# Performance work log

Hardware: AMD Instinct MI355X
Metric: run time of the kernel (lower is better)

## Reference

```python
import jax, jax.numpy as jnp
import numpy as np

Z_LOSS_COEF = 0.001
TOP_K = 8


def setup_inputs() -> dict:
    key = jax.random.key(0)
    ks = jax.random.split(key, 8)
    D, L, E, F, FS = 1024, 256, 64, 256, 1024  # d_model, latent, experts, latent d_ff, shared d_ff
    B, S = 1, 1024
    x = jax.random.normal(ks[0], (B, S, D), jnp.float32)
    gate_w = jax.random.normal(ks[1], (E, D), jnp.float32) * 0.01  # router, std=0.01 init
    expert_bias = jnp.zeros((E,), jnp.float32)  # load-balancing bias buffer
    down_w = jax.random.normal(ks[2], (L, D), jnp.float32) * 0.02
    up_w = jax.random.normal(ks[3], (D, L), jnp.float32) * 0.02
    shared_gu_w = jax.random.normal(ks[4], (2 * FS, D), jnp.float32) * 0.02
    shared_down_w = jax.random.normal(ks[5], (D, FS), jnp.float32) * 0.02
    exp_gu_w = jax.random.normal(ks[6], (E, L, 2 * F), jnp.float32) * 0.02  # [E,K,N] layout
    exp_down_w = jax.random.normal(ks[7], (E, F, L), jnp.float32) * 0.02
    return {"x": x, "gate_w": gate_w, "expert_bias": expert_bias,
            "down_w": down_w, "up_w": up_w,
            "shared_gu_w": shared_gu_w, "shared_down_w": shared_down_w,
            "exp_gu_w": exp_gu_w, "exp_down_w": exp_down_w}


def reference(x, gate_w, expert_bias, down_w, up_w, shared_gu_w, shared_down_w, exp_gu_w, exp_down_w):
    B, S, D = x.shape
    xf = x.reshape(-1, D)                     # [N, D]
    N = xf.shape[0]
    E = gate_w.shape[0]
    # ---- AuxLossFreeRouter (full d_model input) ----
    logits = xf @ gate_w.T                    # [N, E]
    z_loss = Z_LOSS_COEF * jnp.mean(jax.nn.logsumexp(logits, axis=-1) ** 2)
    affinity = jax.nn.sigmoid(logits)
    scores = affinity + expert_bias           # bias only affects selection, not weights
    _, sel = jax.lax.top_k(scores, TOP_K)     # [N, K] int32
    sel_aff = jnp.take_along_axis(affinity, sel, axis=1)
    gw = sel_aff / (sel_aff.sum(-1, keepdims=True) + 1e-9)  # [N, K]
    # sparse combine matrix [N, E]
    combine = jnp.zeros((N, E), xf.dtype).at[jnp.arange(N)[:, None], sel].add(gw)
    # ---- shared SwiGLU expert at full d_model ----
    sh = xf @ shared_gu_w.T
    g, u = jnp.split(sh, 2, axis=-1)
    shared_out = (jax.nn.silu(g) * u) @ shared_down_w.T     # [N, D]
    # ---- latent batched experts: down-project, dense-over-E SwiGLU, sparse combine ----
    lat = xf @ down_w.T                       # [N, L]
    h = jnp.einsum('nl,elf->nef', lat, exp_gu_w)            # [N, E, 2F]
    hg, hu = jnp.split(h, 2, axis=-1)
    hid = jax.nn.silu(hg) * hu                # [N, E, F]
    y = jnp.einsum('nef,efl->nel', hid, exp_down_w)         # [N, E, L]
    routed_lat = jnp.einsum('ne,nel->nl', combine, y)       # sparse top-k combine
    routed = routed_lat @ up_w.T              # [N, D]
    out = (shared_out + routed).reshape(B, S, D)
    return out, z_loss
```

## Files before the change

### kernel.cpp

```cpp
#include <hip/hip_runtime.h>
#include <stdint.h>


using f32x4 = __attribute__((ext_vector_type(4))) float;
using s16x8 = __attribute__((ext_vector_type(8))) short;

#define MFMA_BF16(a, b, c) __builtin_amdgcn_mfma_f32_16x16x32_bf16((a), (b), (c), 0, 0, 0)

__device__ __forceinline__ unsigned short f2bf(float f) {
  union { float f; uint32_t u; } v; v.f = f;
  uint32_t u = v.u;
  u += 0x7FFFu + ((u >> 16) & 1u);
  return (unsigned short)(u >> 16);
}
__device__ __forceinline__ float bf2f(unsigned short h) {
  union { uint32_t u; float f; } v; v.u = ((uint32_t)h) << 16;
  return v.f;
}
__device__ __forceinline__ float silu_f(float x) { return x / (1.f + expf(-x)); }

__device__ __forceinline__ void cvt16(const float* __restrict__ src,
                                      unsigned short* __restrict__ dst) {
  if (src) {
#pragma unroll
    for (int i = 0; i < 4; ++i) {
      float4 v = *(const float4*)(src + i * 4);
      *(ushort4*)(dst + i * 4) =
          make_ushort4(f2bf(v.x), f2bf(v.y), f2bf(v.z), f2bf(v.w));
    }
  } else {
#pragma unroll
    for (int i = 0; i < 4; ++i) *(ushort4*)(dst + i * 4) = make_ushort4(0, 0, 0, 0);
  }
}

struct PackArgs {
  const float *x, *gate, *down, *sgu, *sdw, *up, *egu, *edw;
  unsigned short *xb, *Wcat, *Bf, *egut, *edwt;
  int* counts;
  float* zp;
};

__global__ void pack_kernel(PackArgs a) {
  __shared__ float tile[32][33];
  const int b = blockIdx.x, t = threadIdx.x;
  if (b == 0) {
    if (t < 64) a.counts[t] = 0;
    if (t == 64) *a.zp = 0.f;
  }
  if (b < 608) {
    const int r = b * 4 + (t >> 6), c = (t & 63) * 16;
    const float* src;
    if (r < 64)       src = a.gate + (size_t)r * 1024 + c;
    else if (r < 320) src = a.down + (size_t)(r - 64) * 1024 + c;
    else if (r < 384) src = nullptr;
    else {
      const int i = r - 384;
      src = a.sgu + (size_t)((i >> 1) + (i & 1) * 1024) * 1024 + c;
    }
    cvt16(src, a.Wcat + (size_t)r * 1024 + c);
  } else if (b < 928) {
    const int idx = (b - 608) * 4096 + t * 16;
    const int row = idx / 1280, col = idx - row * 1280;
    const float* src = (col < 1024) ? a.sdw + (size_t)row * 1024 + col
                                    : a.up + (size_t)row * 256 + (col - 1024);
    cvt16(src, a.Bf + idx);
  } else if (b < 1184) {
    const int idx = (b - 928) * 4096 + t * 16;
    cvt16(a.x + idx, a.xb + idx);
  } else {
    const float* src; unsigned short* dst; int lds, tr, tc; bool inter;
    if (b < 9376) {
      const int q = b - 1184, e = q >> 7, tt = q & 127;
      tr = tt >> 4; tc = tt & 15; lds = 512; inter = true;
      src = a.egu + (size_t)e * 131072; dst = a.egut + (size_t)e * 131072;
    } else {
      const int q = b - 9376, e = q >> 6, tt = q & 63;
      tr = tt >> 3; tc = tt & 7; lds = 256; inter = false;
      src = a.edw + (size_t)e * 65536; dst = a.edwt + (size_t)e * 65536;
    }
    const int r = t >> 3, c4 = (t & 7) * 4;
    float4 v = *(const float4*)(src + (size_t)(tr * 32 + r) * lds + tc * 32 + c4);
    tile[r][c4 + 0] = v.x; tile[r][c4 + 1] = v.y;
    tile[r][c4 + 2] = v.z; tile[r][c4 + 3] = v.w;
    __syncthreads();
    const int n = tc * 32 + r;
    const int orow = inter ? ((n < 256) ? 2 * n : 2 * (n - 256) + 1) : n;
    ushort4 o = make_ushort4(f2bf(tile[c4 + 0][r]), f2bf(tile[c4 + 1][r]),
                             f2bf(tile[c4 + 2][r]), f2bf(tile[c4 + 3][r]));
    *(ushort4*)(dst + (size_t)orow * 256 + tr * 32 + c4) = o;
  }
}

struct EpiArgs { int mode; void* out; int ldo; int coff; };

__device__ __forceinline__ void stage_tile(const unsigned short* __restrict__ G, int ldg,
                                           int row0, int kt, unsigned short* lbuf,
                                           int wid, int lane) {
#pragma unroll
  for (int j = 0; j < 2; ++j) {
    const int o = j * 4096 + wid * 1024 + lane * 16;
    const int kh = o >> 11;
    const int row = (o & 2047) >> 4;
    const unsigned short* src = G + (size_t)(row0 + row) * ldg + kt * 32 + kh * 8;
    __builtin_amdgcn_global_load_lds(
        (const __attribute__((address_space(1))) void*)src,
        (__attribute__((address_space(3))) void*)(lbuf + (size_t)(j * 2048 + wid * 512)),
        16, 0, 0);
  }
}

__device__ __forceinline__ void wave_fence() { asm volatile("" ::: "memory"); }

__device__ __forceinline__ void gemm_tile(const unsigned short* __restrict__ A, int lda,
                                          const unsigned short* __restrict__ B, int ldb,
                                          int K, int m0, int n0, EpiArgs epi,
                                          unsigned short* As, unsigned short* Bs) {
  const int tid = threadIdx.x;
  const int wid = tid >> 6, lane = tid & 63;
  const int wm = wid >> 1, wn = wid & 1;

  f32x4 acc[4][4] = {};
  const int NT = K >> 5;

  stage_tile(A, lda, m0, 0, As, wid, lane);
  stage_tile(B, ldb, n0, 0, Bs, wid, lane);
  if (NT > 1) {
    stage_tile(A, lda, m0, 1, As + 4096, wid, lane);
    stage_tile(B, ldb, n0, 1, Bs + 4096, wid, lane);
  }

  const int kh = lane >> 4, r16 = lane & 15;
  int cur = 0;
  for (int kt = 0; kt < NT; ++kt) {
    if (kt + 1 < NT) asm volatile("s_waitcnt vmcnt(4)" ::: "memory");
    else             asm volatile("s_waitcnt vmcnt(0)" ::: "memory");
    wave_fence();
    __builtin_amdgcn_s_barrier();
    wave_fence();

    const unsigned short* Ab = As + cur * 4096;
    const unsigned short* Bb = Bs + cur * 4096;
    s16x8 af[4], bfr[4];
#pragma unroll
    for (int m = 0; m < 4; ++m)
      af[m] = *(const s16x8*)(Ab + kh * 1024 + (wm * 64 + m * 16 + r16) * 8);
#pragma unroll
    for (int n = 0; n < 4; ++n)
      bfr[n] = *(const s16x8*)(Bb + kh * 1024 + (wn * 64 + n * 16 + r16) * 8);

    if (kt + 2 < NT) {
      const int nb = (cur + 2 >= 3) ? cur - 1 : cur + 2;
      stage_tile(A, lda, m0, kt + 2, As + nb * 4096, wid, lane);
      stage_tile(B, ldb, n0, kt + 2, Bs + nb * 4096, wid, lane);
    }

    __builtin_amdgcn_s_setprio(1);
#pragma unroll
    for (int m = 0; m < 4; ++m)
#pragma unroll
      for (int n = 0; n < 4; ++n)
        acc[m][n] = MFMA_BF16(af[m], bfr[n], acc[m][n]);
    __builtin_amdgcn_s_setprio(0);

    cur = (cur + 1 == 3) ? 0 : cur + 1;
  }

#pragma unroll
  for (int m = 0; m < 4; ++m) {
    const int rb = m0 + wm * 64 + m * 16 + (lane >> 4) * 4;
#pragma unroll
    for (int n = 0; n < 4; ++n) {
      const int c = n0 + wn * 64 + n * 16 + (lane & 15);
      if (epi.mode == 0) {
        float* O = (float*)epi.out;
#pragma unroll
        for (int j = 0; j < 4; ++j) O[(size_t)(rb + j) * epi.ldo + c] = acc[m][n][j];
      } else if (epi.mode == 1) {
        unsigned short* O = (unsigned short*)epi.out;
#pragma unroll
        for (int j = 0; j < 4; ++j)
          O[(size_t)(rb + j) * epi.ldo + c] = f2bf(acc[m][n][j]);
      } else {
        unsigned short* O = (unsigned short*)epi.out;
        const int col = (c - epi.coff) >> 1;
#pragma unroll
        for (int j = 0; j < 4; ++j) {
          const float v = acc[m][n][j];
          const float u = __shfl_xor(v, 1);
          if (!(lane & 1))
            O[(size_t)(rb + j) * epi.ldo + col] = f2bf(silu_f(v) * u);
        }
      }
    }
  }
}

__global__ __launch_bounds__(256, 1) void gemm1_kernel(const unsigned short* __restrict__ xb,
                                                       const unsigned short* __restrict__ Wcat,
                                                       float* __restrict__ C1,
                                                       unsigned short* __restrict__ Abuf) {
  __shared__ __align__(16) unsigned short As[3 * 4096];
  __shared__ __align__(16) unsigned short Bs[3 * 4096];
  const int bx = blockIdx.x;
  EpiArgs e;
  if (bx < 3) { e.mode = 0; e.out = C1; e.ldo = 384; e.coff = 0; }
  else        { e.mode = 2; e.out = Abuf; e.ldo = 1280; e.coff = 384; }
  gemm_tile(xb, 1024, Wcat, 1024, 1024, blockIdx.y * 128, bx * 128, e, As, Bs);
}

__global__ __launch_bounds__(256, 1) void gemm_final(const unsigned short* __restrict__ Abuf,
                                                     const unsigned short* __restrict__ Bf,
                                                     float* __restrict__ out) {
  __shared__ __align__(16) unsigned short As[3 * 4096];
  __shared__ __align__(16) unsigned short Bs[3 * 4096];
  EpiArgs e; e.mode = 0; e.out = out; e.ldo = 1024; e.coff = 0;
  gemm_tile(Abuf, 1280, Bf, 1280, 1280, blockIdx.y * 128, blockIdx.x * 128, e, As, Bs);
}

__global__ __launch_bounds__(256, 1) void gemm_grouped(const unsigned short* __restrict__ A0,
                                                       const unsigned short* __restrict__ B0,
                                                       int Bstride, EpiArgs epi, int K,
                                                       const int* __restrict__ counts) {
  const int e = blockIdx.y >> 1, rt = blockIdx.y & 1;
  int cnt = counts[e];
  if (cnt > 256) cnt = 256;
  if (rt * 128 >= cnt) return;
  __shared__ __align__(16) unsigned short As[3 * 4096];
  __shared__ __align__(16) unsigned short Bs[3 * 4096];
  const int base = e * 256 + rt * 128;
  epi.out = (void*)((unsigned short*)epi.out + (size_t)base * epi.ldo);
  gemm_tile(A0 + (size_t)base * K, K, B0 + (size_t)e * Bstride, K, K, 0,
            blockIdx.x * 128, epi, As, Bs);
}

__global__ void router_kernel(const float* __restrict__ C1,
                              const float* __restrict__ bias,
                              unsigned short* __restrict__ lat_g,
                              int* __restrict__ counts,
                              int* __restrict__ slot_nk, float* __restrict__ gw_nk,
                              float* __restrict__ zp) {
  const int n = blockIdx.x * 4 + (threadIdx.x >> 6);
  const int lane = threadIdx.x & 63;
  const float* row = C1 + (size_t)n * 384;
  const float logit = row[lane];

  float mx = logit;
#pragma unroll
  for (int d = 32; d; d >>= 1) mx = fmaxf(mx, __shfl_xor(mx, d));
  float se = expf(logit - mx);
#pragma unroll
  for (int d = 32; d; d >>= 1) se += __shfl_xor(se, d);
  if (lane == 0) {
    const float lse = mx + logf(se);
    atomicAdd(zp, 0.001f * lse * lse * (1.f / 1024.f));
  }

  const float aff = 1.f / (1.f + expf(-logit));
  float s = aff + bias[lane];

  float asum = 0.f;
  int e_mine = 0; float a_mine = 0.f;
#pragma unroll
  for (int k = 0; k < 8; ++k) {
    float m2 = s;
#pragma unroll
    for (int d = 32; d; d >>= 1) m2 = fmaxf(m2, __shfl_xor(m2, d));
    const unsigned long long blt = __ballot(s == m2);
    const int idx = __ffsll(blt) - 1;
    const float a = __shfl(aff, idx);
    asum += a;
    if (lane == k) { e_mine = idx; a_mine = a; }
    if (lane == idx) s = -3.0e38f;
  }
  const float inv = 1.f / (asum + 1e-9f);

  int slot = 0;
  if (lane < 8) {
    int pos = atomicAdd(&counts[e_mine], 1);
    if (pos > 255) pos = 255;
    slot = e_mine * 256 + pos;
    slot_nk[(size_t)n * 8 + lane] = slot;
    gw_nk[(size_t)n * 8 + lane] = a_mine * inv;
  }

  const float4 lv = *(const float4*)(row + 64 + lane * 4);
  const ushort4 lb = make_ushort4(f2bf(lv.x), f2bf(lv.y), f2bf(lv.z), f2bf(lv.w));
#pragma unroll
  for (int k = 0; k < 8; ++k) {
    const int sl = __shfl(slot, k);
    *(ushort4*)(lat_g + (size_t)sl * 256 + lane * 4) = lb;
  }
}

__global__ void combine_kernel(const unsigned short* __restrict__ y,
                               const int* __restrict__ slot_nk,
                               const float* __restrict__ gw_nk,
                               unsigned short* __restrict__ Abuf) {
  const int n = blockIdx.x * 4 + (threadIdx.x >> 6);
  const int l4 = (threadIdx.x & 63) * 4;
  float a0 = 0.f, a1 = 0.f, a2 = 0.f, a3 = 0.f;
#pragma unroll
  for (int k = 0; k < 8; ++k) {
    const int sl = slot_nk[(size_t)n * 8 + k];
    const float g = gw_nk[(size_t)n * 8 + k];
    const ushort4 yv = *(const ushort4*)(y + (size_t)sl * 256 + l4);
    a0 += g * bf2f(yv.x); a1 += g * bf2f(yv.y);
    a2 += g * bf2f(yv.z); a3 += g * bf2f(yv.w);
  }
  *(ushort4*)(Abuf + (size_t)n * 1280 + 1024 + l4) =
      make_ushort4(f2bf(a0), f2bf(a1), f2bf(a2), f2bf(a3));
}

extern "C" void kernel_launch(void* const* d_in, const int* in_sizes, int n_in,
                              void* d_out, int out_size, void* d_ws, size_t ws_size,
                              hipStream_t stream) {
  (void)in_sizes; (void)n_in; (void)out_size; (void)ws_size;
  const float* x      = (const float*)d_in[0];
  const float* gate_w = (const float*)d_in[1];
  const float* bias   = (const float*)d_in[2];
  const float* down_w = (const float*)d_in[3];
  const float* up_w   = (const float*)d_in[4];
  const float* sgu    = (const float*)d_in[5];
  const float* sdw    = (const float*)d_in[6];
  const float* egu    = (const float*)d_in[7];
  const float* edw    = (const float*)d_in[8];
  float* out = (float*)d_out;

  char* w = (char*)d_ws;
  auto alloc = [&](size_t bytes) { char* p = w; w += (bytes + 255) & ~(size_t)255; return p; };
  unsigned short* xb    = (unsigned short*)alloc(1048576ull * 2);
  unsigned short* Wcat  = (unsigned short*)alloc(2432ull * 1024 * 2);
  unsigned short* Bf    = (unsigned short*)alloc(1024ull * 1280 * 2);
  unsigned short* egut  = (unsigned short*)alloc(64ull * 512 * 256 * 2);
  unsigned short* edwt  = (unsigned short*)alloc(64ull * 256 * 256 * 2);
  float*          C1    = (float*)alloc(1024ull * 384 * 4);
  unsigned short* Abuf  = (unsigned short*)alloc(1024ull * 1280 * 2);
  unsigned short* lat_g = (unsigned short*)alloc(16384ull * 256 * 2);
  unsigned short* hide  = (unsigned short*)alloc(16384ull * 256 * 2);
  unsigned short* ybuf  = (unsigned short*)alloc(16384ull * 256 * 2);
  int*   counts  = (int*)alloc(64 * 4);
  int*   slot_nk = (int*)alloc(8192 * 4);
  float* gw_nk   = (float*)alloc(8192 * 4);

  PackArgs pa;
  pa.x = x; pa.gate = gate_w; pa.down = down_w; pa.sgu = sgu; pa.sdw = sdw;
  pa.up = up_w; pa.egu = egu; pa.edw = edw;
  pa.xb = xb; pa.Wcat = Wcat; pa.Bf = Bf; pa.egut = egut; pa.edwt = edwt;
  pa.counts = counts; pa.zp = out + 1048576;
  pack_kernel<<<dim3(13472), dim3(256), 0, stream>>>(pa);

  gemm1_kernel<<<dim3(19, 8), dim3(256), 0, stream>>>(xb, Wcat, C1, Abuf);

  router_kernel<<<dim3(256), dim3(256), 0, stream>>>(
      C1, bias, lat_g, counts, slot_nk, gw_nk, out + 1048576);

  {
    EpiArgs e; e.mode = 2; e.out = hide; e.ldo = 256; e.coff = 0;
    gemm_grouped<<<dim3(4, 128), dim3(256), 0, stream>>>(
        lat_g, egut, 512 * 256, e, 256, counts);
  }

  {
    EpiArgs e; e.mode = 1; e.out = ybuf; e.ldo = 256; e.coff = 0;
    gemm_grouped<<<dim3(2, 128), dim3(256), 0, stream>>>(
        hide, edwt, 256 * 256, e, 256, counts);
  }

  combine_kernel<<<dim3(256), dim3(256), 0, stream>>>(ybuf, slot_nk, gw_nk, Abuf);

  gemm_final<<<dim3(8, 8), dim3(256), 0, stream>>>(Abuf, Bf, out);
}
```

Baseline: 140.1 us.

## Fuse all stages into one persistent kernel with software grid barriers

Merges the pack, gemm1, router, both grouped expert GEMMs, combine and final GEMM into a single persistent kernel of 256 blocks, separated by atomic-counter grid barriers. It also replaces the z-loss atomicAdd with per-token lse² storage and a block reduction. The aim is to remove the launch gaps between seven kernels. The cost is fewer blocks per phase: the pack phase runs as a 256-block strided loop, the grouped GEMMs get fewer concurrent blocks, and every barrier adds spin-wait time. Progress also relies on all 256 blocks being co-resident.

```diff
diff --git a/kernel.cpp b/kernel.cpp
--- a/kernel.cpp
+++ b/kernel.cpp
@@ -34,20 +34,33 @@
   }
 }
 
-struct PackArgs {
-  const float *x, *gate, *down, *sgu, *sdw, *up, *egu, *edw;
-  unsigned short *xb, *Wcat, *Bf, *egut, *edwt;
-  int* counts;
-  float* zp;
+union SMem {
+  float tp[32][33];
+  struct { unsigned short As[3 * 4096]; unsigned short Bs[3 * 4096]; } g;
 };
 
-__global__ void pack_kernel(PackArgs a) {
-  __shared__ float tile[32][33];
-  const int b = blockIdx.x, t = threadIdx.x;
-  if (b == 0) {
-    if (t < 64) a.counts[t] = 0;
-    if (t == 64) *a.zp = 0.f;
-  }
+struct MegaArgs {
+  const float *x, *gate, *down, *sgu, *sdw, *up, *egu, *edw, *bias;
+  unsigned short *xb, *Wcat, *Bf, *egut, *edwt, *Abuf, *lat_g, *hide, *ybuf;
+  float *C1, *lse2, *out;
+  int *counts, *slot_nk;
+  float *gw_nk;
+  int *bars;
+};
+
+__device__ __forceinline__ void grid_barrier(int* bar, int nblk) {
+  __syncthreads();
+  if (threadIdx.x == 0) {
+    __threadfence();
+    __hip_atomic_fetch_add(bar, 1, __ATOMIC_RELEASE, __HIP_MEMORY_SCOPE_AGENT);
+    while (__hip_atomic_load(bar, __ATOMIC_ACQUIRE, __HIP_MEMORY_SCOPE_AGENT) < nblk)
+      __builtin_amdgcn_s_sleep(2);
+    __threadfence();
+  }
+  __syncthreads();
+}
+
+__device__ void pack_unit(int b, int t, const MegaArgs& a, SMem& sm) {
   if (b < 608) {
     const int r = b * 4 + (t >> 6), c = (t & 63) * 16;
     const float* src;
@@ -81,14 +94,15 @@
     }
     const int r = t >> 3, c4 = (t & 7) * 4;
     float4 v = *(const float4*)(src + (size_t)(tr * 32 + r) * lds + tc * 32 + c4);
-    tile[r][c4 + 0] = v.x; tile[r][c4 + 1] = v.y;
-    tile[r][c4 + 2] = v.z; tile[r][c4 + 3] = v.w;
+    sm.tp[r][c4 + 0] = v.x; sm.tp[r][c4 + 1] = v.y;
+    sm.tp[r][c4 + 2] = v.z; sm.tp[r][c4 + 3] = v.w;
     __syncthreads();
     const int n = tc * 32 + r;
     const int orow = inter ? ((n < 256) ? 2 * n : 2 * (n - 256) + 1) : n;
-    ushort4 o = make_ushort4(f2bf(tile[c4 + 0][r]), f2bf(tile[c4 + 1][r]),
-                             f2bf(tile[c4 + 2][r]), f2bf(tile[c4 + 3][r]));
+    ushort4 o = make_ushort4(f2bf(sm.tp[c4 + 0][r]), f2bf(sm.tp[c4 + 1][r]),
+                             f2bf(sm.tp[c4 + 2][r]), f2bf(sm.tp[c4 + 3][r]));
     *(ushort4*)(dst + (size_t)orow * 256 + tr * 32 + c4) = o;
+    __syncthreads();
   }
 }
 
@@ -112,10 +126,11 @@
 
 __device__ __forceinline__ void wave_fence() { asm volatile("" ::: "memory"); }
 
-__device__ __forceinline__ void gemm_tile(const unsigned short* __restrict__ A, int lda,
-                                          const unsigned short* __restrict__ B, int ldb,
-                                          int K, int m0, int n0, EpiArgs epi,
-                                          unsigned short* As, unsigned short* Bs) {
+__device__ void gemm_tile(const unsigned short* __restrict__ A, int lda,
+                          const unsigned short* __restrict__ B, int ldb,
+                          int K, int m0, int n0, EpiArgs epi,
+                          unsigned short* As, unsigned short* Bs) {
+  __syncthreads();
   const int tid = threadIdx.x;
   const int wid = tid >> 6, lane = tid & 63;
   const int wm = wid >> 1, wn = wid & 1;
@@ -196,53 +211,10 @@
   }
 }
 
-__global__ __launch_bounds__(256, 1) void gemm1_kernel(const unsigned short* __restrict__ xb,
-                                                       const unsigned short* __restrict__ Wcat,
-                                                       float* __restrict__ C1,
-                                                       unsigned short* __restrict__ Abuf) {
-  __shared__ __align__(16) unsigned short As[3 * 4096];
-  __shared__ __align__(16) unsigned short Bs[3 * 4096];
-  const int bx = blockIdx.x;
-  EpiArgs e;
-  if (bx < 3) { e.mode = 0; e.out = C1; e.ldo = 384; e.coff = 0; }
-  else        { e.mode = 2; e.out = Abuf; e.ldo = 1280; e.coff = 384; }
-  gemm_tile(xb, 1024, Wcat, 1024, 1024, blockIdx.y * 128, bx * 128, e, As, Bs);
-}
-
-__global__ __launch_bounds__(256, 1) void gemm_final(const unsigned short* __restrict__ Abuf,
-                                                     const unsigned short* __restrict__ Bf,
-                                                     float* __restrict__ out) {
-  __shared__ __align__(16) unsigned short As[3 * 4096];
-  __shared__ __align__(16) unsigned short Bs[3 * 4096];
-  EpiArgs e; e.mode = 0; e.out = out; e.ldo = 1024; e.coff = 0;
-  gemm_tile(Abuf, 1280, Bf, 1280, 1280, blockIdx.y * 128, blockIdx.x * 128, e, As, Bs);
-}
-
-__global__ __launch_bounds__(256, 1) void gemm_grouped(const unsigned short* __restrict__ A0,
-                                                       const unsigned short* __restrict__ B0,
-                                                       int Bstride, EpiArgs epi, int K,
-                                                       const int* __restrict__ counts) {
-  const int e = blockIdx.y >> 1, rt = blockIdx.y & 1;
-  int cnt = counts[e];
-  if (cnt > 256) cnt = 256;
-  if (rt * 128 >= cnt) return;
-  __shared__ __align__(16) unsigned short As[3 * 4096];
-  __shared__ __align__(16) unsigned short Bs[3 * 4096];
-  const int base = e * 256 + rt * 128;
-  epi.out = (void*)((unsigned short*)epi.out + (size_t)base * epi.ldo);
-  gemm_tile(A0 + (size_t)base * K, K, B0 + (size_t)e * Bstride, K, K, 0,
-            blockIdx.x * 128, epi, As, Bs);
-}
-
-__global__ void router_kernel(const float* __restrict__ C1,
-                              const float* __restrict__ bias,
-                              unsigned short* __restrict__ lat_g,
-                              int* __restrict__ counts,
-                              int* __restrict__ slot_nk, float* __restrict__ gw_nk,
-                              float* __restrict__ zp) {
-  const int n = blockIdx.x * 4 + (threadIdx.x >> 6);
-  const int lane = threadIdx.x & 63;
-  const float* row = C1 + (size_t)n * 384;
+__device__ void router_block(int b, int tid, const MegaArgs& a) {
+  const int n = b * 4 + (tid >> 6);
+  const int lane = tid & 63;
+  const float* row = a.C1 + (size_t)n * 384;
   const float logit = row[lane];
 
   float mx = logit;
@@ -253,11 +225,11 @@
   for (int d = 32; d; d >>= 1) se += __shfl_xor(se, d);
   if (lane == 0) {
     const float lse = mx + logf(se);
-    atomicAdd(zp, 0.001f * lse * lse * (1.f / 1024.f));
+    a.lse2[n] = lse * lse;
   }
 
   const float aff = 1.f / (1.f + expf(-logit));
-  float s = aff + bias[lane];
+  float s = aff + a.bias[lane];
 
   float asum = 0.f;
   int e_mine = 0; float a_mine = 0.f;
@@ -268,20 +240,20 @@
     for (int d = 32; d; d >>= 1) m2 = fmaxf(m2, __shfl_xor(m2, d));
     const unsigned long long blt = __ballot(s == m2);
     const int idx = __ffsll(blt) - 1;
-    const float a = __shfl(aff, idx);
-    asum += a;
-    if (lane == k) { e_mine = idx; a_mine = a; }
+    const float af_ = __shfl(aff, idx);
+    asum += af_;
+    if (lane == k) { e_mine = idx; a_mine = af_; }
     if (lane == idx) s = -3.0e38f;
   }
   const float inv = 1.f / (asum + 1e-9f);
 
   int slot = 0;
   if (lane < 8) {
-    int pos = atomicAdd(&counts[e_mine], 1);
+    int pos = atomicAdd(&a.counts[e_mine], 1);
     if (pos > 255) pos = 255;
     slot = e_mine * 256 + pos;
-    slot_nk[(size_t)n * 8 + lane] = slot;
-    gw_nk[(size_t)n * 8 + lane] = a_mine * inv;
+    a.slot_nk[(size_t)n * 8 + lane] = slot;
+    a.gw_nk[(size_t)n * 8 + lane] = a_mine * inv;
   }
 
   const float4 lv = *(const float4*)(row + 64 + lane * 4);
@@ -289,85 +261,134 @@
 #pragma unroll
   for (int k = 0; k < 8; ++k) {
     const int sl = __shfl(slot, k);
-    *(ushort4*)(lat_g + (size_t)sl * 256 + lane * 4) = lb;
-  }
-}
-
-__global__ void combine_kernel(const unsigned short* __restrict__ y,
-                               const int* __restrict__ slot_nk,
-                               const float* __restrict__ gw_nk,
-                               unsigned short* __restrict__ Abuf) {
-  const int n = blockIdx.x * 4 + (threadIdx.x >> 6);
-  const int l4 = (threadIdx.x & 63) * 4;
+    *(ushort4*)(a.lat_g + (size_t)sl * 256 + lane * 4) = lb;
+  }
+}
+
+__device__ void combine_block(int b, int tid, const MegaArgs& a, SMem& sm) {
+  const int n = b * 4 + (tid >> 6);
+  const int l4 = (tid & 63) * 4;
   float a0 = 0.f, a1 = 0.f, a2 = 0.f, a3 = 0.f;
 #pragma unroll
   for (int k = 0; k < 8; ++k) {
-    const int sl = slot_nk[(size_t)n * 8 + k];
-    const float g = gw_nk[(size_t)n * 8 + k];
-    const ushort4 yv = *(const ushort4*)(y + (size_t)sl * 256 + l4);
+    const int sl = a.slot_nk[(size_t)n * 8 + k];
+    const float g = a.gw_nk[(size_t)n * 8 + k];
+    const ushort4 yv = *(const ushort4*)(a.ybuf + (size_t)sl * 256 + l4);
     a0 += g * bf2f(yv.x); a1 += g * bf2f(yv.y);
     a2 += g * bf2f(yv.z); a3 += g * bf2f(yv.w);
   }
-  *(ushort4*)(Abuf + (size_t)n * 1280 + 1024 + l4) =
+  *(ushort4*)(a.Abuf + (size_t)n * 1280 + 1024 + l4) =
       make_ushort4(f2bf(a0), f2bf(a1), f2bf(a2), f2bf(a3));
+
+  if (b == 0) {
+    __syncthreads();
+    float s = a.lse2[tid] + a.lse2[tid + 256] + a.lse2[tid + 512] + a.lse2[tid + 768];
+    ((float*)sm.tp)[tid] = s;
+    __syncthreads();
+    for (int d = 128; d; d >>= 1) {
+      if (tid < d) ((float*)sm.tp)[tid] += ((float*)sm.tp)[tid + d];
+      __syncthreads();
+    }
+    if (tid == 0) a.out[1048576] = 0.001f * ((float*)sm.tp)[0] * (1.f / 1024.f);
+  }
+}
+
+__global__ __launch_bounds__(256, 1) void moe_mega(MegaArgs a) {
+  __shared__ SMem sm;
+  const int b = blockIdx.x, tid = threadIdx.x;
+
+  if (b == 0 && tid < 64) a.counts[tid] = 0;
+  for (int u = b; u < 13472; u += 256) pack_unit(u, tid, a, sm);
+  grid_barrier(a.bars + 0, 256);
+
+  if (b < 152) {
+    const int bx = b % 19, by = b / 19;
+    EpiArgs e;
+    if (bx < 3) { e.mode = 0; e.out = a.C1; e.ldo = 384; e.coff = 0; }
+    else        { e.mode = 2; e.out = a.Abuf; e.ldo = 1280; e.coff = 384; }
+    gemm_tile(a.xb, 1024, a.Wcat, 1024, 1024, by * 128, bx * 128, e, sm.g.As, sm.g.Bs);
+  }
+  grid_barrier(a.bars + 1, 256);
+
+  router_block(b, tid, a);
+  grid_barrier(a.bars + 2, 256);
+
+  for (int t = b; t < 512; t += 256) {
+    const int xt = t & 3, yt = t >> 2;
+    const int e_ = yt >> 1, rt = yt & 1;
+    int cnt = a.counts[e_];
+    if (cnt > 256) cnt = 256;
+    if (rt * 128 < cnt) {
+      const int base = e_ * 256 + rt * 128;
+      EpiArgs ep; ep.mode = 2; ep.ldo = 256; ep.coff = 0;
+      ep.out = (void*)(a.hide + (size_t)base * 256);
+      gemm_tile(a.lat_g + (size_t)base * 256, 256,
+                a.egut + (size_t)e_ * 131072, 256, 256, 0, xt * 128, ep,
+                sm.g.As, sm.g.Bs);
+    }
+  }
+  grid_barrier(a.bars + 3, 256);
+
+  {
+    const int xt = b & 1, yt = b >> 1;
+    const int e_ = yt >> 1, rt = yt & 1;
+    int cnt = a.counts[e_];
+    if (cnt > 256) cnt = 256;
+    if (rt * 128 < cnt) {
+      const int base = e_ * 256 + rt * 128;
+      EpiArgs ep; ep.mode = 1; ep.ldo = 256; ep.coff = 0;
+      ep.out = (void*)(a.ybuf + (size_t)base * 256);
+      gemm_tile(a.hide + (size_t)base * 256, 256,
+                a.edwt + (size_t)e_ * 65536, 256, 256, 0, xt * 128, ep,
+                sm.g.As, sm.g.Bs);
+    }
+  }
+  grid_barrier(a.bars + 4, 256);
+
+  combine_block(b, tid, a, sm);
+  grid_barrier(a.bars + 5, 256);
+
+  if (b < 64) {
+    EpiArgs e; e.mode = 0; e.out = a.out; e.ldo = 1024; e.coff = 0;
+    gemm_tile(a.Abuf, 1280, a.Bf, 1280, 1280, (b >> 3) * 128, (b & 7) * 128, e,
+              sm.g.As, sm.g.Bs);
+  }
 }
 
 extern "C" void kernel_launch(void* const* d_in, const int* in_sizes, int n_in,
                               void* d_out, int out_size, void* d_ws, size_t ws_size,
                               hipStream_t stream) {
   (void)in_sizes; (void)n_in; (void)out_size; (void)ws_size;
-  const float* x      = (const float*)d_in[0];
-  const float* gate_w = (const float*)d_in[1];
-  const float* bias   = (const float*)d_in[2];
-  const float* down_w = (const float*)d_in[3];
-  const float* up_w   = (const float*)d_in[4];
-  const float* sgu    = (const float*)d_in[5];
-  const float* sdw    = (const float*)d_in[6];
-  const float* egu    = (const float*)d_in[7];
-  const float* edw    = (const float*)d_in[8];
-  float* out = (float*)d_out;
+  MegaArgs a;
+  a.x    = (const float*)d_in[0];
+  a.gate = (const float*)d_in[1];
+  a.bias = (const float*)d_in[2];
+  a.down = (const float*)d_in[3];
+  a.up   = (const float*)d_in[4];
+  a.sgu  = (const float*)d_in[5];
+  a.sdw  = (const float*)d_in[6];
+  a.egu  = (const float*)d_in[7];
+  a.edw  = (const float*)d_in[8];
+  a.out  = (float*)d_out;
 
   char* w = (char*)d_ws;
   auto alloc = [&](size_t bytes) { char* p = w; w += (bytes + 255) & ~(size_t)255; return p; };
-  unsigned short* xb    = (unsigned short*)alloc(1048576ull * 2);
-  unsigned short* Wcat  = (unsigned short*)alloc(2432ull * 1024 * 2);
-  unsigned short* Bf    = (unsigned short*)alloc(1024ull * 1280 * 2);
-  unsigned short* egut  = (unsigned short*)alloc(64ull * 512 * 256 * 2);
-  unsigned short* edwt  = (unsigned short*)alloc(64ull * 256 * 256 * 2);
-  float*          C1    = (float*)alloc(1024ull * 384 * 4);
-  unsigned short* Abuf  = (unsigned short*)alloc(1024ull * 1280 * 2);
-  unsigned short* lat_g = (unsigned short*)alloc(16384ull * 256 * 2);
-  unsigned short* hide  = (unsigned short*)alloc(16384ull * 256 * 2);
-  unsigned short* ybuf  = (unsigned short*)alloc(16384ull * 256 * 2);
-  int*   counts  = (int*)alloc(64 * 4);
-  int*   slot_nk = (int*)alloc(8192 * 4);
-  float* gw_nk   = (float*)alloc(8192 * 4);
-
-  PackArgs pa;
-  pa.x = x; pa.gate = gate_w; pa.down = down_w; pa.sgu = sgu; pa.sdw = sdw;
-  pa.up = up_w; pa.egu = egu; pa.edw = edw;
-  pa.xb = xb; pa.Wcat = Wcat; pa.Bf = Bf; pa.egut = egut; pa.edwt = edwt;
-  pa.counts = counts; pa.zp = out + 1048576;
-  pack_kernel<<<dim3(13472), dim3(256), 0, stream>>>(pa);
-
-  gemm1_kernel<<<dim3(19, 8), dim3(256), 0, stream>>>(xb, Wcat, C1, Abuf);
-
-  router_kernel<<<dim3(256), dim3(256), 0, stream>>>(
-      C1, bias, lat_g, counts, slot_nk, gw_nk, out + 1048576);
-
-  {
-    EpiArgs e; e.mode = 2; e.out = hide; e.ldo = 256; e.coff = 0;
-    gemm_grouped<<<dim3(4, 128), dim3(256), 0, stream>>>(
-        lat_g, egut, 512 * 256, e, 256, counts);
-  }
-
-  {
-    EpiArgs e; e.mode = 1; e.out = ybuf; e.ldo = 256; e.coff = 0;
-    gemm_grouped<<<dim3(2, 128), dim3(256), 0, stream>>>(
-        hide, edwt, 256 * 256, e, 256, counts);
-  }
-
-  combine_kernel<<<dim3(256), dim3(256), 0, stream>>>(ybuf, slot_nk, gw_nk, Abuf);
-
-  gemm_final<<<dim3(8, 8), dim3(256), 0, stream>>>(Abuf, Bf, out);
-}
+  a.xb    = (unsigned short*)alloc(1048576ull * 2);
+  a.Wcat  = (unsigned short*)alloc(2432ull * 1024 * 2);
+  a.Bf    = (unsigned short*)alloc(1024ull * 1280 * 2);
+  a.egut  = (unsigned short*)alloc(64ull * 512 * 256 * 2);
+  a.edwt  = (unsigned short*)alloc(64ull * 256 * 256 * 2);
+  a.C1    = (float*)alloc(1024ull * 384 * 4);
+  a.Abuf  = (unsigned short*)alloc(1024ull * 1280 * 2);
+  a.lat_g = (unsigned short*)alloc(16384ull * 256 * 2);
+  a.hide  = (unsigned short*)alloc(16384ull * 256 * 2);
+  a.ybuf  = (unsigned short*)alloc(16384ull * 256 * 2);
+  a.lse2  = (float*)alloc(1024 * 4);
+  a.counts  = (int*)alloc(64 * 4);
+  a.slot_nk = (int*)alloc(8192 * 4);
+  a.gw_nk   = (float*)alloc(8192 * 4);
+  a.bars    = (int*)alloc(16 * 4);
+
+  hipMemsetAsync(a.bars, 0, 16 * 4, stream);
+  moe_mega<<<dim3(256), dim3(256), 0, stream>>>(a);
+}
```

New measurement: 383.1 us. 2.74x slower.
